# Kernel optimization log

Measured on AMD Instinct MI355X. Metric: run time of the kernel, lower is better.

Reference implementation:

```python
import jax, jax.numpy as jnp
import numpy as np

B, IDF, RES = 32, 64, 128
CDF, SRC_L, A_DIM = 768, 18, 100
QUERY_L = RES * RES


def setup_inputs() -> dict:
    key = jax.random.key(0)
    ks = jax.random.split(key, 5)
    inputs = jax.random.normal(ks[0], (B, IDF, RES, RES), dtype=jnp.float32)
    context = jax.random.normal(ks[1], (B, CDF, SRC_L), dtype=jnp.float32)
    conv_ctx_w = jax.random.normal(ks[2], (IDF, CDF), dtype=jnp.float32) * (1.0 / np.sqrt(CDF))
    conv_w = jax.random.normal(ks[3], (IDF,), dtype=jnp.float32) * (1.0 / np.sqrt(IDF))
    conv_b = jnp.zeros((1,), dtype=jnp.float32)
    fc_w = jax.random.normal(ks[4], (A_DIM, QUERY_L), dtype=jnp.float32) * (1.0 / np.sqrt(QUERY_L))
    fc_b = jnp.zeros((A_DIM,), dtype=jnp.float32)
    return {"inputs": inputs, "context": context, "conv_ctx_w": conv_ctx_w,
            "conv_w": conv_w, "conv_b": conv_b, "fc_w": fc_w, "fc_b": fc_b}


def reference(inputs, context, conv_ctx_w, conv_w, conv_b, fc_w, fc_b):
    b, idf, ih, iw = inputs.shape
    queryL = ih * iw
    # target: [b, idf, queryL]
    target = inputs.reshape(b, idf, queryL)
    # 1x1 conv on context (conv_context): [b, idf, sourceL]
    sourceT = jnp.einsum('ic,bcs->bis', conv_ctx_w, context)
    # attn scores: [b, queryL, sourceL]; softmax over sourceL (dim=1 on flattened view)
    attn = jnp.einsum('biq,bis->bqs', target, sourceT)
    attn = jax.nn.softmax(attn, axis=-1)
    # weighted context: [b, idf, queryL]
    wctx = jnp.einsum('bis,bqs->biq', sourceT, attn)
    # 1x1 conv to single channel (self.conv): [b, queryL]
    wctx = jnp.einsum('i,biq->bq', conv_w, wctx) + conv_b
    # att_fc: [b, a_dim]
    out = wctx @ fc_w.T + fc_b
    return out
```

## Files before the change

kernel.cpp:

```cpp
#include <hip/hip_runtime.h>

#define BB 32
#define IDF 64
#define QL 16384
#define CDF 768
#define SL 18
#define SLP 20
#define CLP 21
#define ADIM 100

__global__ __launch_bounds__(256, 2) void kA_source(
        const float* __restrict__ ctx,
        const float* __restrict__ wic,
        const float* __restrict__ fc_b,
        float* __restrict__ sT,
        float* __restrict__ out)
{
    __shared__ float ctx_l[CDF * CLP];
    const int blk  = blockIdx.x;
    const int tid  = threadIdx.x;
    const int wave = tid >> 6;
    const int lane = tid & 63;
    const int b = blk >> 4;
    const int g = blk & 15;

    if (blk < 13) {
        const int t = blk * 256 + tid;
        if (t < BB * ADIM) out[t] = fc_b[t % ADIM];
    }

    const float* ctxb = ctx + (size_t)b * CDF * SL;
    for (int t = tid; t < CDF * SL; t += 256) {
        const int c = t / SL;
        const int s = t - c * SL;
        ctx_l[c * CLP + s] = ctxb[t];
    }
    __syncthreads();

    const int i = g * 4 + wave;
    const float* wrow = wic + (size_t)i * CDF;

    float acc[SL];
#pragma unroll
    for (int s = 0; s < SL; s++) acc[s] = 0.f;

#pragma unroll 2
    for (int k = 0; k < CDF / 64; k++) {
        const int c = k * 64 + lane;
        const float wv = wrow[c];
#pragma unroll
        for (int s = 0; s < SL; s++) acc[s] += wv * ctx_l[c * CLP + s];
    }
#pragma unroll
    for (int s = 0; s < SL; s++) {
        float a = acc[s];
#pragma unroll
        for (int off = 32; off; off >>= 1) a += __shfl_xor(a, off, 64);
        if (lane == 0) sT[((size_t)b * IDF + i) * SLP + s] = a;
    }
}

__global__ __launch_bounds__(256, 2) void kB_attn(
        const float* __restrict__ inp,
        const float* __restrict__ sT,
        const float* __restrict__ conv_w,
        const float* __restrict__ conv_b,
        float* __restrict__ wq)
{
    __shared__ float v_l[SL];
    const int b   = blockIdx.y;
    const int qt  = blockIdx.x;
    const int tid = threadIdx.x;
    const float* st = sT + (size_t)b * IDF * SLP;

    if (tid < SL) {
        float a = 0.f;
        for (int i = 0; i < IDF; i++) a += conv_w[i] * st[i * SLP + tid];
        v_l[tid] = a;
    }
    __syncthreads();

    const float2* ip2 = (const float2*)(inp + (size_t)b * IDF * QL + (size_t)qt * 512);

    float2 sc[SL];
#pragma unroll
    for (int s = 0; s < SL; s++) sc[s] = make_float2(0.f, 0.f);

    float2 xb[4];
#pragma unroll
    for (int j = 0; j < 4; j++) xb[j] = ip2[(size_t)j * (QL / 2) + tid];

#pragma unroll 4
    for (int i = 0; i < IDF; i++) {
        const float2 x = xb[i & 3];
        if (i + 4 < IDF) xb[i & 3] = ip2[(size_t)(i + 4) * (QL / 2) + tid];
        const float* strow = st + i * SLP;
#pragma unroll
        for (int s = 0; s < SL; s++) {
            const float rs = strow[s];
            sc[s].x += x.x * rs;
            sc[s].y += x.y * rs;
        }
    }

    float2 m = sc[0];
#pragma unroll
    for (int s = 1; s < SL; s++) {
        m.x = fmaxf(m.x, sc[s].x);
        m.y = fmaxf(m.y, sc[s].y);
    }
    float2 l = make_float2(0.f, 0.f);
    float2 o = make_float2(0.f, 0.f);
#pragma unroll
    for (int s = 0; s < SL; s++) {
        const float vs = v_l[s];
        float2 p;
        p.x = __expf(sc[s].x - m.x);
        p.y = __expf(sc[s].y - m.y);
        l.x += p.x; l.y += p.y;
        o.x += p.x * vs; o.y += p.y * vs;
    }
    const float cb = conv_b[0];
    float2 res;
    res.x = o.x / l.x + cb;
    res.y = o.y / l.y + cb;
    ((float2*)(wq + (size_t)b * QL + (size_t)qt * 512))[tid] = res;
}

__global__ __launch_bounds__(320, 2) void kC_fc(
        const float* __restrict__ wq,
        const float* __restrict__ fcw,
        float* __restrict__ out)
{
    const int blk = blockIdx.x;
    const int bg  = blk / 80;
    const int rem = blk - bg * 80;
    const int ag  = rem >> 3;
    const int qc  = rem & 7;
    const int wave = threadIdx.x >> 6;
    const int lane = threadIdx.x & 63;
    const int a0 = ag * 10 + wave * 2;
    const int b0 = bg * 8;
    const int q0 = qc * 2048;

    float acc[2][8];
#pragma unroll
    for (int j = 0; j < 2; j++)
#pragma unroll
        for (int i = 0; i < 8; i++) acc[j][i] = 0.f;

#pragma unroll 2
    for (int k = 0; k < 8; k++) {
        const int qi = q0 + (k * 64 + lane) * 4;
        float4 fv[2];
#pragma unroll
        for (int j = 0; j < 2; j++) fv[j] = *(const float4*)(fcw + (size_t)(a0 + j) * QL + qi);
        float4 wv[8];
#pragma unroll
        for (int i = 0; i < 8; i++) wv[i] = *(const float4*)(wq + (size_t)(b0 + i) * QL + qi);
#pragma unroll
        for (int j = 0; j < 2; j++)
#pragma unroll
            for (int i = 0; i < 8; i++)
                acc[j][i] += fv[j].x * wv[i].x + fv[j].y * wv[i].y
                           + fv[j].z * wv[i].z + fv[j].w * wv[i].w;
    }

#pragma unroll
    for (int j = 0; j < 2; j++) {
#pragma unroll
        for (int i = 0; i < 8; i++) {
            float r = acc[j][i];
#pragma unroll
            for (int off = 32; off; off >>= 1) r += __shfl_xor(r, off, 64);
            if (lane == 0) atomicAdd(&out[(b0 + i) * ADIM + a0 + j], r);
        }
    }
}

extern "C" void kernel_launch(void* const* d_in, const int* in_sizes, int n_in,
                              void* d_out, int out_size, void* d_ws, size_t ws_size,
                              hipStream_t stream)
{
    const float* inputs     = (const float*)d_in[0];
    const float* context    = (const float*)d_in[1];
    const float* conv_ctx_w = (const float*)d_in[2];
    const float* conv_w     = (const float*)d_in[3];
    const float* conv_b     = (const float*)d_in[4];
    const float* fc_w       = (const float*)d_in[5];
    const float* fc_b       = (const float*)d_in[6];
    float* out = (float*)d_out;

    float* ws = (float*)d_ws;
    float* sT = ws;
    float* wq = ws + (size_t)BB * IDF * SLP;

    kA_source<<<dim3(512), dim3(256), 0, stream>>>(context, conv_ctx_w, fc_b, sT, out);
    kB_attn<<<dim3(32, BB), dim3(256), 0, stream>>>(inputs, sT, conv_w, conv_b, wq);
    kC_fc<<<dim3(320), dim3(320), 0, stream>>>(wq, fc_w, out);
}
```

Measured before the change: 238.6 us.

## Stage attention input tiles into LDS via async global_load_lds double buffering

The attention kernel stops loading each input channel row into registers with a four-deep software prefetch. It now streams 8-row chunks of the input tile straight into a double-buffered LDS array using the direct global-to-LDS load builtin, with one barrier per chunk, and reads operands from LDS. Launch bounds are raised to 4 blocks per CU to hide more memory latency. The costs are 32KB of LDS per block and a reliance on the barrier waiting for the async loads to finish. Each thread now owns columns tid and tid+256 instead of an adjacent pair, so its output stores become two scalar writes.

```diff
diff --git a/kernel.cpp b/kernel.cpp
--- a/kernel.cpp
+++ b/kernel.cpp
@@ -9,6 +9,9 @@
 #define CLP 21
 #define ADIM 100
 
+typedef __attribute__((address_space(3))) unsigned int lds_u32_t;
+typedef __attribute__((address_space(1))) const unsigned int glb_u32_t;
+
 __global__ __launch_bounds__(256, 2) void kA_source(
         const float* __restrict__ ctx,
         const float* __restrict__ wic,
@@ -60,17 +63,20 @@
     }
 }
 
-__global__ __launch_bounds__(256, 2) void kB_attn(
+__global__ __launch_bounds__(256, 4) void kB_attn(
         const float* __restrict__ inp,
         const float* __restrict__ sT,
         const float* __restrict__ conv_w,
         const float* __restrict__ conv_b,
         float* __restrict__ wq)
 {
+    __shared__ __align__(16) float xbuf[2][8][512];
     __shared__ float v_l[SL];
     const int b   = blockIdx.y;
     const int qt  = blockIdx.x;
     const int tid = threadIdx.x;
+    const int wave = tid >> 6;
+    const int lane = tid & 63;
     const float* st = sT + (size_t)b * IDF * SLP;
 
     if (tid < SL) {
@@ -78,28 +84,45 @@
         for (int i = 0; i < IDF; i++) a += conv_w[i] * st[i * SLP + tid];
         v_l[tid] = a;
     }
-    __syncthreads();
-
-    const float2* ip2 = (const float2*)(inp + (size_t)b * IDF * QL + (size_t)qt * 512);
+
+    const float* gbase = inp + (size_t)b * IDF * QL + (size_t)qt * 512;
+
+#define STAGE(st_idx, buf)                                                              \
+    {                                                                                   \
+        const int i0_ = (st_idx) * 8;                                                   \
+        _Pragma("unroll")                                                               \
+        for (int c_ = 0; c_ < 4; c_++) {                                                \
+            const int j_ = wave * 4 + c_;                                               \
+            const int r_ = j_ >> 1, h_ = j_ & 1;                                        \
+            const float* g_ = gbase + (size_t)(i0_ + r_) * QL + h_ * 256 + lane * 4;    \
+            float* l_ = &xbuf[(buf)][r_][h_ * 256];                                     \
+            __builtin_amdgcn_global_load_lds((glb_u32_t*)g_, (lds_u32_t*)l_, 16, 0, 0); \
+        }                                                                               \
+    }
+
+    STAGE(0, 0);
 
     float2 sc[SL];
 #pragma unroll
     for (int s = 0; s < SL; s++) sc[s] = make_float2(0.f, 0.f);
 
-    float2 xb[4];
-#pragma unroll
-    for (int j = 0; j < 4; j++) xb[j] = ip2[(size_t)j * (QL / 2) + tid];
-
-#pragma unroll 4
-    for (int i = 0; i < IDF; i++) {
-        const float2 x = xb[i & 3];
-        if (i + 4 < IDF) xb[i & 3] = ip2[(size_t)(i + 4) * (QL / 2) + tid];
-        const float* strow = st + i * SLP;
-#pragma unroll
-        for (int s = 0; s < SL; s++) {
-            const float rs = strow[s];
-            sc[s].x += x.x * rs;
-            sc[s].y += x.y * rs;
+#pragma unroll 1
+    for (int k = 0; k < 8; k++) {
+        __syncthreads();
+        if (k < 7) STAGE(k + 1, (k + 1) & 1);
+        const int kb = k & 1;
+#pragma unroll
+        for (int r = 0; r < 8; r++) {
+            const int i = k * 8 + r;
+            const float x0 = xbuf[kb][r][tid];
+            const float x1 = xbuf[kb][r][tid + 256];
+            const float* strow = st + i * SLP;
+#pragma unroll
+            for (int s = 0; s < SL; s++) {
+                const float rs = strow[s];
+                sc[s].x += x0 * rs;
+                sc[s].y += x1 * rs;
+            }
         }
     }
 
@@ -121,10 +144,9 @@
         o.x += p.x * vs; o.y += p.y * vs;
     }
     const float cb = conv_b[0];
-    float2 res;
-    res.x = o.x / l.x + cb;
-    res.y = o.y / l.y + cb;
-    ((float2*)(wq + (size_t)b * QL + (size_t)qt * 512))[tid] = res;
+    float* wqb = wq + (size_t)b * QL + (size_t)qt * 512;
+    wqb[tid]       = o.x / l.x + cb;
+    wqb[tid + 256] = o.y / l.y + cb;
 }
 
 __global__ __launch_bounds__(320, 2) void kC_fc(
```

Result: no change. 234.8 us (-1.6%).
